# Performance work log

Measured on AMD Instinct MI355X. Metric: run time of the kernel, lower is better.

Reference implementation:

```python
import jax, jax.numpy as jnp
import numpy as np

NUM_CLASSES = 80
D_IMG = 2048
D_WORD = 300
D_MID = 1024
B = 8
CONV = 14


def setup_inputs() -> dict:
    key = jax.random.key(0)
    ks = jax.random.split(key, 6)
    s = lambda k, shape, sc: jax.random.normal(k, shape, dtype=jnp.float32) * sc
    return {
        "batch_size": B,
        "img_feature_map": jax.random.normal(ks[0], (B, D_IMG, CONV, CONV), dtype=jnp.float32),
        "word_features": jax.random.normal(ks[1], (NUM_CLASSES, D_WORD), dtype=jnp.float32),
        "W1": s(ks[2], (D_MID, D_IMG), 0.02),
        "W2": s(ks[3], (D_MID, D_WORD), 0.02),
        "W3": s(ks[4], (D_MID, D_MID), 0.02),
        "b3": jnp.zeros((D_MID,), jnp.float32),
        "Wa": s(ks[5], (1, D_MID), 0.02),
        "ba": jnp.zeros((1,), jnp.float32),
    }


def reference(batch_size, img_feature_map, word_features, W1, W2, W3, b3, Wa, ba):
    # img_feature_map: [B, D_img, H, W] -> [B, H, W, D_img] (matches torch double transpose)
    Bn, D, H, W = img_feature_map.shape
    fmap = jnp.transpose(img_feature_map, (0, 2, 3, 1))                 # [B,H,W,D]
    f_wh = jnp.einsum('bhwd,md->bhwm', fmap, W1)                        # fc_1: [B,H,W,M]
    f_wd = word_features @ W2.T                                         # fc_2: [C,M]
    # broadcast multiply (no explicit repeat) + tanh
    t = jnp.tanh(f_wh[:, :, :, None, :] * f_wd)                         # [B,H,W,C,M]
    lb = jnp.einsum('bhwcm,nm->bhwcn', t, W3) + b3                      # fc_3: [B,H,W,C,M]
    coef = jnp.einsum('bhwcm,m->bhwc', lb, Wa[0]) + ba[0]               # fc_a: [B,H,W,C]
    # softmax over spatial positions per (batch, class)
    C = coef.shape[-1]
    coef = jax.nn.softmax(coef.reshape(Bn, H * W, C), axis=1).reshape(Bn, H, W, C)
    # softmax-weighted spatial pooling -> [B, C, D]
    return jnp.einsum('bhwc,bhwd->bcd', coef, fmap)
```

## Files before the change

kernel.cpp:

```cpp
#include <hip/hip_runtime.h>
#include <hip/hip_bf16.h>
#include <stdint.h>

#define NB 8
#define DIMG 2048
#define HWN 196
#define PN 1568
#define DMID 1024
#define NC 80
#define DWORD 300
#define PART 8
#define KSPLIT 4

typedef short bf16x8 __attribute__((ext_vector_type(8)));
typedef float f32x4 __attribute__((ext_vector_type(4)));

__device__ __forceinline__ unsigned short f2bf(float x) {
  union { float f; unsigned u; } c; c.f = x;
  unsigned r = c.u + 0x7FFFu + ((c.u >> 16) & 1u);
  return (unsigned short)(r >> 16);
}

__global__ void k_tc(const float* __restrict__ img, unsigned short* __restrict__ fmapH,
                     const float* __restrict__ W1, unsigned short* __restrict__ W1h) {
  __shared__ float tile[64][33];
  int bx = blockIdx.x;
  int tx = threadIdx.x, ty = threadIdx.y;
  if (bx < 1792) {
    int d0 = (bx & 31) * 64;
    int rem = bx >> 5;
    int h0 = (rem % 7) * 32, b = rem / 7;
    const float* src = img + (size_t)b * DIMG * HWN;
#pragma unroll
    for (int i = 0; i < 64; i += 8) {
      int hw = h0 + tx;
      tile[ty + i][tx] = (hw < HWN) ? src[(size_t)(d0 + ty + i) * HWN + hw] : 0.f;
    }
    __syncthreads();
#pragma unroll
    for (int i = 0; i < 32; i += 8) {
      int hw = h0 + ty + i;
      if (hw < HWN) {
        int d = tx * 2;
        unsigned short lo = f2bf(tile[d][ty + i]);
        unsigned short hi = f2bf(tile[d + 1][ty + i]);
        unsigned v = (unsigned)lo | ((unsigned)hi << 16);
        *(unsigned*)&fmapH[(size_t)(b * HWN + hw) * DIMG + d0 + d] = v;
      }
    }
  } else {
    int tid = ty * 32 + tx;
    int i = ((bx - 1792) * 256 + tid) * 4;
    f32x4 v = *(const f32x4*)(W1 + i);
    ushort4 s;
    s.x = f2bf(v[0]); s.y = f2bf(v[1]); s.z = f2bf(v[2]); s.w = f2bf(v[3]);
    *(ushort4*)(W1h + i) = s;
  }
}

#define GLDS(g, l) \
  __builtin_amdgcn_global_load_lds((const __attribute__((address_space(1))) void*)(g), \
                                   (__attribute__((address_space(3))) void*)(l), 16, 0, 0)

__global__ __launch_bounds__(256) void k_gw(const unsigned short* __restrict__ A,
                                            const unsigned short* __restrict__ Bw,
                                            float* __restrict__ C,
                                            const float* __restrict__ word,
                                            const float* __restrict__ W2,
                                            float* __restrict__ fwd,
                                            const float* __restrict__ Wa,
                                            const float* __restrict__ W3,
                                            float* __restrict__ partial) {
  __shared__ __align__(16) char smem[38400];
  int bz = blockIdx.x;
  int t = threadIdx.x;
  if (bz < 416) {
    unsigned short* As = (unsigned short*)smem;
    unsigned short* Bs = As + 4096;
    int m0 = (bz % 13) * 128;
    int n0 = ((bz / 13) & 7) * 128;
    int koff = (bz / 104) * 512;
    int w = t >> 6, l = t & 63;
    int wr = w >> 1, wc = w & 1;
    f32x4 zero = {0.f, 0.f, 0.f, 0.f};
    f32x4 acc[4][4];
#pragma unroll
    for (int i = 0; i < 4; ++i)
#pragma unroll
      for (int j = 0; j < 4; ++j) acc[i][j] = zero;

    int sr = t >> 2, sk = (t & 3) << 3;
    const unsigned short* ga0 = A + (size_t)(m0 + sr) * 2048 + koff + sk;
    const unsigned short* ga1 = A + (size_t)(m0 + 64 + sr) * 2048 + koff + sk;
    const unsigned short* gb0 = Bw + (size_t)(n0 + sr) * 2048 + koff + sk;
    const unsigned short* gb1 = Bw + (size_t)(n0 + 64 + sr) * 2048 + koff + sk;

    int fr = l & 15, ko = (l >> 4) << 3;

    for (int kk = 0; kk < 512; kk += 32) {
      __syncthreads();
      GLDS(ga0 + kk, As + t * 8);
      GLDS(ga1 + kk, As + t * 8 + 2048);
      GLDS(gb0 + kk, Bs + t * 8);
      GLDS(gb1 + kk, Bs + t * 8 + 2048);
      __syncthreads();
      bf16x8 a[4], b[4];
#pragma unroll
      for (int i = 0; i < 4; ++i)
        a[i] = *(const bf16x8*)&As[(wr * 64 + i * 16 + fr) * 32 + ko];
#pragma unroll
      for (int j = 0; j < 4; ++j)
        b[j] = *(const bf16x8*)&Bs[(wc * 64 + j * 16 + fr) * 32 + ko];
#pragma unroll
      for (int i = 0; i < 4; ++i)
#pragma unroll
        for (int j = 0; j < 4; ++j)
          acc[i][j] = __builtin_amdgcn_mfma_f32_16x16x32_bf16(a[i], b[j], acc[i][j], 0, 0, 0);
    }
    float* Cz = C + (size_t)(bz / 104) * (1600 * DMID);
    int cr = (l >> 4) << 2, cc2 = l & 15;
#pragma unroll
    for (int i = 0; i < 4; ++i) {
#pragma unroll
      for (int q = 0; q < 4; ++q) {
        int row = m0 + wr * 64 + i * 16 + cr + q;
        if (row < 1600) {
#pragma unroll
          for (int j = 0; j < 4; ++j)
            Cz[(size_t)row * DMID + n0 + wc * 64 + j * 16 + cc2] = acc[i][j][q];
        }
      }
    }
  } else if (bz < 736) {
    float* w2s = (float*)smem;
    float* wds = w2s + 16 * 300;
    int idx = bz - 416;
    int m0 = (idx & 63) * 16, c0 = (idx >> 6) * 16;
    const float SC = 2.8853900817779268f;
    for (int u = t; u < 16 * 75; u += 256) {
      int r = u / 75, q = u - r * 75;
      *(f32x4*)&w2s[r * 300 + q * 4] = *(const f32x4*)(W2 + (size_t)(m0 + r) * DWORD + q * 4);
      f32x4 v = *(const f32x4*)(word + (size_t)(c0 + r) * DWORD + q * 4);
      *(f32x4*)&wds[r * 300 + q * 4] = v * SC;
    }
    __syncthreads();
    int ci = t >> 4, mi = t & 15;
    f32x4 av = {0.f, 0.f, 0.f, 0.f};
    const float* wr_ = &wds[ci * 300];
    const float* w2r = &w2s[mi * 300];
    for (int q = 0; q < 75; ++q) {
      f32x4 wv = *(const f32x4*)&wr_[q * 4];
      f32x4 bv = *(const f32x4*)&w2r[q * 4];
#pragma unroll
      for (int u = 0; u < 4; ++u) av[u] = fmaf(wv[u], bv[u], av[u]);
    }
    fwd[(size_t)(c0 + ci) * DMID + m0 + mi] = av[0] + av[1] + av[2] + av[3];
  } else {
    int idx = bz - 736;
    int m = (idx & 3) * 256 + t;
    int n0 = (idx >> 2) * 64;
    float acc = 0.f;
#pragma unroll 4
    for (int n = n0; n < n0 + 64; ++n) acc = fmaf(Wa[n], W3[(size_t)n * DMID + m], acc);
    partial[(size_t)(idx >> 2) * DMID + m] = acc;
  }
}

#define MC 64
__global__ __launch_bounds__(256) void k_coef(const float* __restrict__ fwhp,
                                              const float* __restrict__ fwd,
                                              const float* __restrict__ partial,
                                              float* __restrict__ coefp) {
  __shared__ __align__(16) float al[32][68];
  __shared__ __align__(16) float bl[16][68];
  __shared__ __align__(16) float wl[MC];
  int p0 = blockIdx.x * 32, c0 = blockIdx.y * 16, mz = blockIdx.z;
  int t = threadIdx.x;
  int pi = t >> 4, ci = t & 15;
  float acc[2] = {0.f, 0.f};
  const size_t FS = (size_t)1600 * DMID;

  for (int mc = 0; mc < 2; ++mc) {
    int mbase = mz * 128 + mc * MC;
    __syncthreads();
    {
      int sra = t >> 3, sca = (t & 7) << 3;
      const float* gA = fwhp + (size_t)(p0 + sra) * DMID + mbase + sca;
#pragma unroll
      for (int q = 0; q < 2; ++q) {
        f32x4 v = *(const f32x4*)&gA[q * 4];
        v += *(const f32x4*)&gA[FS + q * 4];
        v += *(const f32x4*)&gA[2 * FS + q * 4];
        v += *(const f32x4*)&gA[3 * FS + q * 4];
        *(f32x4*)&al[sra][sca + q * 4] = v;
      }
      int srb = t >> 4, scb = (t & 15) << 2;
      *(f32x4*)&bl[srb][scb] = *(const f32x4*)(fwd + (size_t)(c0 + srb) * DMID + mbase + scb);
      if (t < MC) {
        float v = 0.f;
#pragma unroll
        for (int s = 0; s < 16; ++s) v += partial[(size_t)s * DMID + mbase + t];
        wl[t] = -2.f * v;
      }
    }
    __syncthreads();
    for (int mm = 0; mm < MC; mm += 4) {
      f32x4 wv = *(const f32x4*)&wl[mm];
      f32x4 bv = *(const f32x4*)&bl[ci][mm];
      f32x4 av0 = *(const f32x4*)&al[pi][mm];
      f32x4 av1 = *(const f32x4*)&al[pi + 16][mm];
#pragma unroll
      for (int u = 0; u < 4; ++u) {
        float w = wv[u], b = bv[u];
        float e0 = __builtin_amdgcn_exp2f(av0[u] * b);
        float e1 = __builtin_amdgcn_exp2f(av1[u] * b);
        acc[0] = fmaf(w, __builtin_amdgcn_rcpf(1.f + e0), acc[0]);
        acc[1] = fmaf(w, __builtin_amdgcn_rcpf(1.f + e1), acc[1]);
      }
    }
  }
  float* cp = coefp + (size_t)mz * (PN * NC);
#pragma unroll
  for (int j = 0; j < 2; ++j) {
    int p = p0 + pi + 16 * j;
    if (p < PN) cp[(size_t)p * NC + c0 + ci] = acc[j];
  }
}

__global__ __launch_bounds__(256) void k_pool(const float* __restrict__ coefp,
                                              const float* __restrict__ img,
                                              float* __restrict__ out) {
  __shared__ __align__(16) float wt[HWN][16];
  __shared__ float red[16][16];
  __shared__ float mxs[16], inv[16];
  int dc = blockIdx.x * 256, cg = blockIdx.y * 16, b = blockIdx.z;
  int t = threadIdx.x;
  for (int i = t; i < HWN * 4; i += 256) {
    int hw = i >> 2, j4 = (i & 3) << 2;
    size_t o = (size_t)(b * HWN + hw) * NC + cg + j4;
    f32x4 s = {0.f, 0.f, 0.f, 0.f};
#pragma unroll
    for (int z = 0; z < PART; ++z) s += *(const f32x4*)&coefp[o + (size_t)z * (PN * NC)];
    *(f32x4*)&wt[hw][j4] = s;
  }
  __syncthreads();
  int j = t & 15, g = t >> 4;
  float pm = -1e30f;
  for (int hw = g; hw < HWN; hw += 16) pm = fmaxf(pm, wt[hw][j]);
  red[g][j] = pm;
  __syncthreads();
  if (t < 16) {
    float m = red[0][t];
#pragma unroll
    for (int g2 = 1; g2 < 16; ++g2) m = fmaxf(m, red[g2][t]);
    mxs[t] = m;
  }
  __syncthreads();
  float mj = mxs[j], ps = 0.f;
  for (int hw = g; hw < HWN; hw += 16) {
    float e = __builtin_amdgcn_exp2f((wt[hw][j] - mj) * 1.4426950408889634f);
    wt[hw][j] = e;
    ps += e;
  }
  red[g][j] = ps;
  __syncthreads();
  if (t < 16) {
    float s = 0.f;
#pragma unroll
    for (int g2 = 0; g2 < 16; ++g2) s += red[g2][t];
    inv[t] = 1.f / s;
  }
  __syncthreads();
  float acc[16];
#pragma unroll
  for (int q = 0; q < 16; ++q) acc[q] = 0.f;
  const float* fpd = img + ((size_t)b * DIMG + dc + t) * HWN;
  for (int hw = 0; hw < HWN; ++hw) {
    float v = fpd[hw];
#pragma unroll
    for (int q = 0; q < 16; ++q) acc[q] = fmaf(wt[hw][q], v, acc[q]);
  }
#pragma unroll
  for (int q = 0; q < 16; ++q)
    out[((size_t)b * NC + cg + q) * DIMG + dc + t] = acc[q] * inv[q];
}

extern "C" void kernel_launch(void* const* d_in, const int* in_sizes, int n_in,
                              void* d_out, int out_size, void* d_ws, size_t ws_size,
                              hipStream_t stream) {
  const float* img  = (const float*)d_in[1];
  const float* word = (const float*)d_in[2];
  const float* W1   = (const float*)d_in[3];
  const float* W2   = (const float*)d_in[4];
  const float* W3   = (const float*)d_in[5];
  const float* Wa   = (const float*)d_in[7];
  float* out = (float*)d_out;
  char* ws = (char*)d_ws;

  unsigned short* fmapH   = (unsigned short*)(ws + 0);
  unsigned short* W1h     = (unsigned short*)(ws + 6815744);
  float*          fwhp    = (float*)(ws + 11010048);
  float*          fwd     = (float*)(ws + 37224448);
  float*          partial = (float*)(ws + 37617664);
  float*          coefp   = (float*)(ws + 37683200);

  hipLaunchKernelGGL(k_tc, dim3(3840), dim3(32, 8), 0, stream, img, fmapH, W1, W1h);
  hipLaunchKernelGGL(k_gw, dim3(800), dim3(256), 0, stream,
                     fmapH, W1h, fwhp, word, W2, fwd, Wa, W3, partial);
  hipLaunchKernelGGL(k_coef, dim3(49, 5, 8), dim3(256), 0, stream, fwhp, fwd, partial, coefp);
  hipLaunchKernelGGL(k_pool, dim3(8, 5, 8), dim3(256), 0, stream, coefp, img, out);
  (void)in_sizes; (void)n_in; (void)out_size; (void)ws_size;
}
```

Before: 100.2 us.

## Halve GEMM k-split and M-partitions, pool from transposed fp32 feature map

```diff
diff --git a/kernel.cpp b/kernel.cpp
--- a/kernel.cpp
+++ b/kernel.cpp
@@ -9,11 +9,11 @@
 #define DMID 1024
 #define NC 80
 #define DWORD 300
-#define PART 8
-#define KSPLIT 4
+#define PART 4
 
 typedef short bf16x8 __attribute__((ext_vector_type(8)));
 typedef float f32x4 __attribute__((ext_vector_type(4)));
+typedef float f32x2 __attribute__((ext_vector_type(2)));
 
 __device__ __forceinline__ unsigned short f2bf(float x) {
   union { float f; unsigned u; } c; c.f = x;
@@ -21,7 +21,8 @@
   return (unsigned short)(r >> 16);
 }
 
-__global__ void k_tc(const float* __restrict__ img, unsigned short* __restrict__ fmapH,
+__global__ void k_tc(const float* __restrict__ img, float* __restrict__ fmap,
+                     unsigned short* __restrict__ fmapH,
                      const float* __restrict__ W1, unsigned short* __restrict__ W1h) {
   __shared__ float tile[64][33];
   int bx = blockIdx.x;
@@ -42,10 +43,12 @@
       int hw = h0 + ty + i;
       if (hw < HWN) {
         int d = tx * 2;
-        unsigned short lo = f2bf(tile[d][ty + i]);
-        unsigned short hi = f2bf(tile[d + 1][ty + i]);
-        unsigned v = (unsigned)lo | ((unsigned)hi << 16);
-        *(unsigned*)&fmapH[(size_t)(b * HWN + hw) * DIMG + d0 + d] = v;
+        float v0 = tile[d][ty + i], v1 = tile[d + 1][ty + i];
+        size_t o = (size_t)(b * HWN + hw) * DIMG + d0 + d;
+        f32x2 fv = {v0, v1};
+        *(f32x2*)&fmap[o] = fv;
+        unsigned hv = (unsigned)f2bf(v0) | ((unsigned)f2bf(v1) << 16);
+        *(unsigned*)&fmapH[o] = hv;
       }
     }
   } else {
@@ -74,12 +77,12 @@
   __shared__ __align__(16) char smem[38400];
   int bz = blockIdx.x;
   int t = threadIdx.x;
-  if (bz < 416) {
+  if (bz < 208) {
     unsigned short* As = (unsigned short*)smem;
     unsigned short* Bs = As + 4096;
     int m0 = (bz % 13) * 128;
     int n0 = ((bz / 13) & 7) * 128;
-    int koff = (bz / 104) * 512;
+    int koff = (bz / 104) * 1024;
     int w = t >> 6, l = t & 63;
     int wr = w >> 1, wc = w & 1;
     f32x4 zero = {0.f, 0.f, 0.f, 0.f};
@@ -97,7 +100,7 @@
 
     int fr = l & 15, ko = (l >> 4) << 3;
 
-    for (int kk = 0; kk < 512; kk += 32) {
+    for (int kk = 0; kk < 1024; kk += 32) {
       __syncthreads();
       GLDS(ga0 + kk, As + t * 8);
       GLDS(ga1 + kk, As + t * 8 + 2048);
@@ -131,10 +134,10 @@
         }
       }
     }
-  } else if (bz < 736) {
+  } else if (bz < 528) {
     float* w2s = (float*)smem;
     float* wds = w2s + 16 * 300;
-    int idx = bz - 416;
+    int idx = bz - 208;
     int m0 = (idx & 63) * 16, c0 = (idx >> 6) * 16;
     const float SC = 2.8853900817779268f;
     for (int u = t; u < 16 * 75; u += 256) {
@@ -156,7 +159,7 @@
     }
     fwd[(size_t)(c0 + ci) * DMID + m0 + mi] = av[0] + av[1] + av[2] + av[3];
   } else {
-    int idx = bz - 736;
+    int idx = bz - 528;
     int m = (idx & 3) * 256 + t;
     int n0 = (idx >> 2) * 64;
     float acc = 0.f;
@@ -180,8 +183,8 @@
   float acc[2] = {0.f, 0.f};
   const size_t FS = (size_t)1600 * DMID;
 
-  for (int mc = 0; mc < 2; ++mc) {
-    int mbase = mz * 128 + mc * MC;
+  for (int mc = 0; mc < 4; ++mc) {
+    int mbase = mz * 256 + mc * MC;
     __syncthreads();
     {
       int sra = t >> 3, sca = (t & 7) << 3;
@@ -190,8 +193,6 @@
       for (int q = 0; q < 2; ++q) {
         f32x4 v = *(const f32x4*)&gA[q * 4];
         v += *(const f32x4*)&gA[FS + q * 4];
-        v += *(const f32x4*)&gA[2 * FS + q * 4];
-        v += *(const f32x4*)&gA[3 * FS + q * 4];
         *(f32x4*)&al[sra][sca + q * 4] = v;
       }
       int srb = t >> 4, scb = (t & 15) << 2;
@@ -228,7 +229,7 @@
 }
 
 __global__ __launch_bounds__(256) void k_pool(const float* __restrict__ coefp,
-                                              const float* __restrict__ img,
+                                              const float* __restrict__ fmap,
                                               float* __restrict__ out) {
   __shared__ __align__(16) float wt[HWN][16];
   __shared__ float red[16][16];
@@ -274,11 +275,19 @@
   float acc[16];
 #pragma unroll
   for (int q = 0; q < 16; ++q) acc[q] = 0.f;
-  const float* fpd = img + ((size_t)b * DIMG + dc + t) * HWN;
-  for (int hw = 0; hw < HWN; ++hw) {
-    float v = fpd[hw];
-#pragma unroll
-    for (int q = 0; q < 16; ++q) acc[q] = fmaf(wt[hw][q], v, acc[q]);
+  const float* fp = fmap + (size_t)b * HWN * DIMG + dc + t;
+  for (int h4 = 0; h4 < HWN / 4; ++h4) {
+    float v0 = fp[(size_t)(h4 * 4 + 0) * DIMG];
+    float v1 = fp[(size_t)(h4 * 4 + 1) * DIMG];
+    float v2 = fp[(size_t)(h4 * 4 + 2) * DIMG];
+    float v3 = fp[(size_t)(h4 * 4 + 3) * DIMG];
+#pragma unroll
+    for (int q = 0; q < 16; ++q) {
+      acc[q] = fmaf(wt[h4 * 4 + 0][q], v0, acc[q]);
+      acc[q] = fmaf(wt[h4 * 4 + 1][q], v1, acc[q]);
+      acc[q] = fmaf(wt[h4 * 4 + 2][q], v2, acc[q]);
+      acc[q] = fmaf(wt[h4 * 4 + 3][q], v3, acc[q]);
+    }
   }
 #pragma unroll
   for (int q = 0; q < 16; ++q)
@@ -297,17 +306,18 @@
   float* out = (float*)d_out;
   char* ws = (char*)d_ws;
 
-  unsigned short* fmapH   = (unsigned short*)(ws + 0);
-  unsigned short* W1h     = (unsigned short*)(ws + 6815744);
-  float*          fwhp    = (float*)(ws + 11010048);
-  float*          fwd     = (float*)(ws + 37224448);
-  float*          partial = (float*)(ws + 37617664);
-  float*          coefp   = (float*)(ws + 37683200);
-
-  hipLaunchKernelGGL(k_tc, dim3(3840), dim3(32, 8), 0, stream, img, fmapH, W1, W1h);
-  hipLaunchKernelGGL(k_gw, dim3(800), dim3(256), 0, stream,
+  float*          fmap    = (float*)(ws + 0);
+  unsigned short* fmapH   = (unsigned short*)(ws + 12845056);
+  unsigned short* W1h     = (unsigned short*)(ws + 19660800);
+  float*          fwhp    = (float*)(ws + 23855104);
+  float*          fwd     = (float*)(ws + 36962304);
+  float*          partial = (float*)(ws + 37355520);
+  float*          coefp   = (float*)(ws + 37421056);
+
+  hipLaunchKernelGGL(k_tc, dim3(3840), dim3(32, 8), 0, stream, img, fmap, fmapH, W1, W1h);
+  hipLaunchKernelGGL(k_gw, dim3(592), dim3(256), 0, stream,
                      fmapH, W1h, fwhp, word, W2, fwd, Wa, W3, partial);
-  hipLaunchKernelGGL(k_coef, dim3(49, 5, 8), dim3(256), 0, stream, fwhp, fwd, partial, coefp);
-  hipLaunchKernelGGL(k_pool, dim3(8, 5, 8), dim3(256), 0, stream, coefp, img, out);
+  hipLaunchKernelGGL(k_coef, dim3(49, 5, 4), dim3(256), 0, stream, fwhp, fwd, partial, coefp);
+  hipLaunchKernelGGL(k_pool, dim3(8, 5, 8), dim3(256), 0, stream, coefp, fmap, out);
   (void)in_sizes; (void)n_in; (void)out_size; (void)ws_size;
 }
```

After: 99.50 us. No clear change (-0.7%).
